# Kernel tuning notes

Measured on AMD Instinct MI355X. Metric: run time of the kernel, lower is better.

## Reference

```python
import jax, jax.numpy as jnp
import numpy as np

B = 8192      # graphs per batch
NPG = 40      # nodes per graph (= average_nodes, uniform here)
DEG = 16      # avg degree
IN = 64
HID = 32
OUT = 10
K1 = 20       # ceil(0.5*40)
K2 = 10       # ceil(0.5*20)
N = B * NPG
E = N * DEG
EPS = 1e-15


def _lin_params(k, fi, fo):
    kw, kb = jax.random.split(k)
    s = 1.0 / np.sqrt(fi)
    w = jax.random.uniform(kw, (fi, fo), jnp.float32, -s, s)
    b = jax.random.uniform(kb, (fo,), jnp.float32, -s, s)
    return w, b


def setup_inputs():
    key = jax.random.key(0)
    ks = jax.random.split(key, 14)
    x = jax.random.normal(ks[0], (N, IN), jnp.float32)
    # edges constrained within each graph (graphs are contiguous blocks of NPG nodes)
    g = jnp.repeat(jnp.arange(B, dtype=jnp.int32), NPG * DEG)
    src = g * NPG + jax.random.randint(ks[1], (E,), 0, NPG, dtype=jnp.int32)
    dst = g * NPG + jax.random.randint(ks[2], (E,), 0, NPG, dtype=jnp.int32)
    edge_index = jnp.stack([src, dst])
    batch = jnp.repeat(jnp.arange(B, dtype=jnp.int32), NPG)
    w_c1, b_c1 = _lin_params(ks[3], IN, HID)
    w_p1, b_p1 = _lin_params(ks[4], HID, K1)
    w2r, b2 = _lin_params(ks[5], HID, HID)
    w2o, _ = _lin_params(ks[6], HID, HID)
    w_p2, b_p2 = _lin_params(ks[7], HID, K2)
    w3r, b3 = _lin_params(ks[8], HID, HID)
    w3o, _ = _lin_params(ks[9], HID, HID)
    w_l1, b_l1 = _lin_params(ks[10], HID, HID)
    w_l2, b_l2 = _lin_params(ks[11], HID, OUT)
    return dict(x=x, edge_index=edge_index, batch=batch,
                w_c1=w_c1, b_c1=b_c1, w_p1=w_p1, b_p1=b_p1,
                w2r=w2r, b2=b2, w2o=w2o, w_p2=w_p2, b_p2=b_p2,
                w3r=w3r, b3=b3, w3o=w3o,
                w_l1=w_l1, b_l1=b_l1, w_l2=w_l2, b_l2=b_l2)


def _gcn_conv(x, edge_index, w, b):
    # PyG GCNConv: x' = D^-1/2 (A + I) D^-1/2 (X W) + b, unit edge weights
    h = x @ w
    row, col = edge_index
    deg = jnp.zeros((N,), h.dtype).at[col].add(1.0) + 1.0  # +1 self loop
    dinv = jax.lax.rsqrt(deg)
    msg = (dinv[row] * dinv[col])[:, None] * h[row]
    out = jnp.zeros_like(h).at[col].add(msg)
    out = out + (dinv * dinv)[:, None] * h  # self-loop contribution
    return out + b


def _dense_mincut_pool(x, adj, s, mask=None):
    # faithful to torch_geometric.nn.dense_mincut_pool
    s = jax.nn.softmax(s, axis=-1)
    if mask is not None:
        m = mask[..., None].astype(x.dtype)
        x = x * m
        s = s * m
    k = s.shape[-1]
    out = jnp.einsum('bnk,bnf->bkf', s, x)
    out_adj = jnp.einsum('bnk,bnm,bml->bkl', s, adj, s)
    mincut_num = jnp.trace(out_adj, axis1=1, axis2=2)
    d_flat = adj.sum(-1)                                   # [B, n]
    mincut_den = jnp.einsum('bnk,bn,bnk->b', s, d_flat, s)  # tr(S^T D S)
    mincut_loss = jnp.mean(-(mincut_num / mincut_den))
    ss = jnp.einsum('bnk,bnl->bkl', s, s)
    ss_norm = jnp.sqrt(jnp.sum(ss * ss, axis=(1, 2), keepdims=True))
    i_s = jnp.eye(k, dtype=x.dtype) / jnp.sqrt(jnp.asarray(k, x.dtype))
    ortho_loss = jnp.mean(jnp.sqrt(jnp.sum((ss / ss_norm - i_s) ** 2, axis=(1, 2))))
    # zero diagonal, then symmetric degree-normalize coarse adjacency
    eye = jnp.eye(k, dtype=x.dtype)
    out_adj = out_adj * (1.0 - eye)
    d = jnp.sqrt(out_adj.sum(-1))[:, None, :] + EPS        # [B,1,k]
    out_adj = out_adj / d / jnp.swapaxes(d, 1, 2)
    return out, out_adj, mincut_loss, ortho_loss


def _dense_graph_conv(x, adj, w_rel, b, w_root):
    # PyG DenseGraphConv (aggr='add'): lin_rel(A @ x) + lin_root(x); lin_root bias=False
    return (adj @ x) @ w_rel + b + x @ w_root


def reference(x, edge_index, batch, w_c1, b_c1, w_p1, b_p1, w2r, b2, w2o,
              w_p2, b_p2, w3r, b3, w3o, w_l1, b_l1, w_l2, b_l2):
    h = jax.nn.relu(_gcn_conv(x, edge_index, w_c1, b_c1))
    # to_dense_batch (uniform NPG nodes per graph, batch sorted)
    local = jnp.arange(N, dtype=jnp.int32) - batch * NPG
    xd = jnp.zeros((B, NPG, HID), h.dtype).at[batch, local].set(h)
    mask = jnp.ones((B, NPG), bool)
    # to_dense_adj (accumulates duplicate edges)
    row, col = edge_index
    g = batch[row]
    adj = jnp.zeros((B, NPG, NPG), h.dtype).at[g, row - g * NPG, col - g * NPG].add(1.0)
    s = xd @ w_p1 + b_p1
    xd, adj, mc1, o1 = _dense_mincut_pool(xd, adj, s, mask)
    xd = jax.nn.relu(_dense_graph_conv(xd, adj, w2r, b2, w2o))
    s = xd @ w_p2 + b_p2
    xd, adj, mc2, o2 = _dense_mincut_pool(xd, adj, s)
    xd = _dense_graph_conv(xd, adj, w3r, b3, w3o)
    pooled = xd.mean(axis=1)
    out = jax.nn.relu(pooled @ w_l1 + b_l1) @ w_l2 + b_l2
    return out, mc1 + mc2 + o1 + o2
```

## Files before the change

### kernel.cpp

```cpp
#include <hip/hip_runtime.h>

#define NT 256

constexpr int Bg   = 8192;
constexpr int NPG  = 40;
constexpr int EPG  = 640;
constexpr int IN_  = 64;
constexpr int HID  = 32;
constexpr int K1   = 20;
constexpr int K2   = 10;
constexpr int OUTC = 10;
constexpr int NE   = Bg * NPG * 16;
constexpr int SX   = 68;
constexpr int SH   = 36;

#define FMA4(acc, a, b) do { \
    acc.x = fmaf((a), (b).x, acc.x); \
    acc.y = fmaf((a), (b).y, acc.y); \
    acc.z = fmaf((a), (b).z, acc.z); \
    acc.w = fmaf((a), (b).w, acc.w); } while (0)

__device__ __forceinline__ float wave_red(float v) {
#pragma unroll
    for (int off = 32; off > 0; off >>= 1) v += __shfl_down(v, off, 64);
    return v;
}

__global__ __launch_bounds__(NT, 4)
void mincut_fused(const float* __restrict__ x, const int* __restrict__ ei,
                  const float* __restrict__ w_c1, const float* __restrict__ b_c1,
                  const float* __restrict__ w_p1, const float* __restrict__ b_p1,
                  const float* __restrict__ w2r_, const float* __restrict__ b2_,
                  const float* __restrict__ w2o_,
                  const float* __restrict__ w_p2, const float* __restrict__ b_p2,
                  const float* __restrict__ w3r_, const float* __restrict__ b3_,
                  const float* __restrict__ w3o_,
                  const float* __restrict__ w_l1, const float* __restrict__ b_l1,
                  const float* __restrict__ w_l2, const float* __restrict__ b_l2,
                  float* __restrict__ out, float* __restrict__ wsg)
{
    __shared__ __align__(16) float sXbuf[NPG * SX];
    __shared__ __align__(16) float sH[NPG * SH];
    __shared__ __align__(16) float sXd[NPG * SH];
    __shared__ __align__(16) float sA[NPG * NPG];
    __shared__ __align__(16) float sA2[K1 * K1];
    __shared__ __align__(16) float sX2[K1 * SH];
    __shared__ __align__(16) float sS2[K1 * K2];
    __shared__ __align__(16) float sX3[K2 * SH];
    __shared__ __align__(16) float sB1[HID];
    __shared__ __align__(16) float sBp1[K1];
    __shared__ __align__(16) float sB2[HID];
    __shared__ __align__(16) float sBp2[K2 + 2];
    __shared__ __align__(16) float sB3[HID];
    __shared__ __align__(16) float sdinv[NPG];
    __shared__ __align__(16) float srowsA[NPG];
    __shared__ __align__(16) float srowm[NPG];
    __shared__ __align__(16) float spool[HID];
    __shared__ __align__(16) float st1[HID];
    __shared__ __align__(16) float sred[4];
    __shared__ __align__(16) float sc[8];

    float* sS  = sXbuf;
    float* sAS = sXbuf + 800;
    float* sSS = sXbuf + 1600;
    float* sA3 = sXbuf + 2000;

    const int g    = blockIdx.x;
    const int tid  = threadIdx.x;
    const int lane = tid & 63;
    const int wid  = tid >> 6;

    int er0, ec0, er1, ec1, er2 = -1, ec2 = 0;
    {
        const int eb = g * EPG, nb = g * NPG;
        const int* srcp = ei;
        const int* dstp = ei + NE;
        int e = eb + tid;
        er0 = srcp[e] - nb; ec0 = dstp[e] - nb;
        e += NT;
        er1 = srcp[e] - nb; ec1 = dstp[e] - nb;
        if (tid + 2 * NT < EPG) {
            e += NT;
            er2 = srcp[e] - nb; ec2 = dstp[e] - nb;
        }
    }
    for (int i = tid; i < NPG * NPG; i += NT) sA[i] = 0.f;
    {
        const float4* xg = (const float4*)(x + (size_t)g * (NPG * IN_));
        for (int i = tid; i < NPG * (IN_ / 4); i += NT) {
            int n = i >> 4, k = i & 15;
            ((float4*)(sXbuf + n * SX))[k] = xg[i];
        }
    }
    if (tid < HID) { sB1[tid] = b_c1[tid]; sB2[tid] = b2_[tid]; sB3[tid] = b3_[tid]; }
    else if (tid >= 64 && tid < 64 + K1)   sBp1[tid - 64]  = b_p1[tid - 64];
    else if (tid >= 128 && tid < 128 + K2) sBp2[tid - 128] = b_p2[tid - 128];
    __syncthreads();

    atomicAdd(&sA[er0 * NPG + ec0], 1.f);
    atomicAdd(&sA[er1 * NPG + ec1], 1.f);
    if (er2 >= 0) atomicAdd(&sA[er2 * NPG + ec2], 1.f);

    if (tid < 160) {
        int np = tid >> 3, fq = tid & 7;
        int n0 = 2 * np, n1 = n0 + 1;
        const float4* a0p = (const float4*)(sXbuf + n0 * SX);
        const float4* a1p = (const float4*)(sXbuf + n1 * SX);
        const float4* wg  = (const float4*)w_c1;
        float4 acc0 = {0.f,0.f,0.f,0.f}, acc1 = {0.f,0.f,0.f,0.f};
#pragma unroll 4
        for (int kk = 0; kk < IN_ / 4; kk++) {
            float4 a0 = a0p[kk], a1 = a1p[kk];
            float4 w0 = wg[(4*kk+0)*8 + fq];
            float4 w1 = wg[(4*kk+1)*8 + fq];
            float4 w2 = wg[(4*kk+2)*8 + fq];
            float4 w3 = wg[(4*kk+3)*8 + fq];
            FMA4(acc0, a0.x, w0); FMA4(acc0, a0.y, w1);
            FMA4(acc0, a0.z, w2); FMA4(acc0, a0.w, w3);
            FMA4(acc1, a1.x, w0); FMA4(acc1, a1.y, w1);
            FMA4(acc1, a1.z, w2); FMA4(acc1, a1.w, w3);
        }
        ((float4*)(sH + n0 * SH))[fq] = acc0;
        ((float4*)(sH + n1 * SH))[fq] = acc1;
    }
    __syncthreads();

    if (tid < NPG) {
        float s = 0.f;
#pragma unroll
        for (int r = 0; r < NPG; r++) s += sA[r * NPG + tid];
        sdinv[tid] = rsqrtf(s + 1.f);
    } else if (tid >= 64 && tid < 64 + NPG) {
        int n = tid - 64; float s = 0.f;
#pragma unroll
        for (int m = 0; m < NPG; m++) s += sA[n * NPG + m];
        srowsA[n] = s;
    }
    __syncthreads();

    if (tid < 160) {
        int cp = tid >> 3, fq = tid & 7;
        int c0 = 2 * cp, c1 = c0 + 1;
        float4 acc0 = {0.f,0.f,0.f,0.f}, acc1 = {0.f,0.f,0.f,0.f};
#pragma unroll 8
        for (int r = 0; r < NPG; r++) {
            float dv = sdinv[r];
            float a0 = sA[r * NPG + c0] * dv;
            float a1 = sA[r * NPG + c1] * dv;
            float4 b = ((const float4*)(sH + r * SH))[fq];
            FMA4(acc0, a0, b);
            FMA4(acc1, a1, b);
        }
        float4 bb = ((const float4*)sB1)[fq];
        float4 h0 = ((const float4*)(sH + c0 * SH))[fq];
        float4 h1 = ((const float4*)(sH + c1 * SH))[fq];
        float d0 = sdinv[c0], d1 = sdinv[c1];
        float4 r0, r1;
        r0.x = fmaxf(fmaf(d0, fmaf(d0, h0.x, acc0.x), bb.x), 0.f);
        r0.y = fmaxf(fmaf(d0, fmaf(d0, h0.y, acc0.y), bb.y), 0.f);
        r0.z = fmaxf(fmaf(d0, fmaf(d0, h0.z, acc0.z), bb.z), 0.f);
        r0.w = fmaxf(fmaf(d0, fmaf(d0, h0.w, acc0.w), bb.w), 0.f);
        r1.x = fmaxf(fmaf(d1, fmaf(d1, h1.x, acc1.x), bb.x), 0.f);
        r1.y = fmaxf(fmaf(d1, fmaf(d1, h1.y, acc1.y), bb.y), 0.f);
        r1.z = fmaxf(fmaf(d1, fmaf(d1, h1.z, acc1.z), bb.z), 0.f);
        r1.w = fmaxf(fmaf(d1, fmaf(d1, h1.w, acc1.w), bb.w), 0.f);
        ((float4*)(sXd + c0 * SH))[fq] = r0;
        ((float4*)(sXd + c1 * SH))[fq] = r1;
    }
    __syncthreads();

    if (tid < 100) {
        int np = tid / 5, lq = tid - np * 5;
        int n0 = 2 * np, n1 = n0 + 1;
        const float4* wg = (const float4*)w_p1;
        float4 bb = ((const float4*)sBp1)[lq];
        float4 acc0 = bb, acc1 = bb;
#pragma unroll 8
        for (int k = 0; k < HID; k++) {
            float a0 = sXd[n0 * SH + k];
            float a1 = sXd[n1 * SH + k];
            float4 w = wg[k * 5 + lq];
            FMA4(acc0, a0, w);
            FMA4(acc1, a1, w);
        }
        ((float4*)(sS + n0 * K1))[lq] = acc0;
        ((float4*)(sS + n1 * K1))[lq] = acc1;
    }
    __syncthreads();

    if (tid < NPG) {
        float* row = sS + tid * K1;
        float v[K1]; float m = -3.0e38f;
#pragma unroll
        for (int k = 0; k < K1; k++) { v[k] = row[k]; m = fmaxf(m, v[k]); }
        float ssum = 0.f;
#pragma unroll
        for (int k = 0; k < K1; k++) { v[k] = __expf(v[k] - m); ssum += v[k]; }
        float inv = 1.f / ssum;
#pragma unroll
        for (int k = 0; k < K1; k++) row[k] = v[k] * inv;
    }
    __syncthreads();

    if (tid < 150) {
        if (tid < 100) {
            int np = tid / 5, lq = tid - np * 5;
            int n0 = 2 * np, n1 = n0 + 1;
            float4 acc0 = {0.f,0.f,0.f,0.f}, acc1 = {0.f,0.f,0.f,0.f};
#pragma unroll 8
            for (int m = 0; m < NPG; m++) {
                float a0 = sA[n0 * NPG + m];
                float a1 = sA[n1 * NPG + m];
                float4 b = ((const float4*)(sS + m * K1))[lq];
                FMA4(acc0, a0, b);
                FMA4(acc1, a1, b);
            }
            ((float4*)(sAS + n0 * K1))[lq] = acc0;
            ((float4*)(sAS + n1 * K1))[lq] = acc1;
        } else {
            int oo = tid - 100;
            int kp = oo / 5, lq = oo - kp * 5;
            int k0 = 2 * kp, k1 = k0 + 1;
            float4 acc0 = {0.f,0.f,0.f,0.f}, acc1 = {0.f,0.f,0.f,0.f};
#pragma unroll 8
            for (int n = 0; n < NPG; n++) {
                float s0 = sS[n * K1 + k0];
                float s1 = sS[n * K1 + k1];
                float4 b = ((const float4*)(sS + n * K1))[lq];
                FMA4(acc0, s0, b);
                FMA4(acc1, s1, b);
            }
            ((float4*)(sSS + k0 * K1))[lq] = acc0;
            ((float4*)(sSS + k1 * K1))[lq] = acc1;
        }
    }
    __syncthreads();

    if (tid < 170) {
        if (tid < 50) {
            int kp = tid / 5, lq = tid - kp * 5;
            int k0 = 2 * kp, k1 = k0 + 1;
            float4 acc0 = {0.f,0.f,0.f,0.f}, acc1 = {0.f,0.f,0.f,0.f};
#pragma unroll 8
            for (int n = 0; n < NPG; n++) {
                float s0 = sS[n * K1 + k0];
                float s1 = sS[n * K1 + k1];
                float4 b = ((const float4*)(sAS + n * K1))[lq];
                FMA4(acc0, s0, b);
                FMA4(acc1, s1, b);
            }
            ((float4*)(sA2 + k0 * K1))[lq] = acc0;
            ((float4*)(sA2 + k1 * K1))[lq] = acc1;
        } else if (tid < 130) {
            int oo = tid - 50;
            int kp = oo >> 3, fq = oo & 7;
            int k0 = 2 * kp, k1 = k0 + 1;
            float4 acc0 = {0.f,0.f,0.f,0.f}, acc1 = {0.f,0.f,0.f,0.f};
#pragma unroll 8
            for (int n = 0; n < NPG; n++) {
                float s0 = sS[n * K1 + k0];
                float s1 = sS[n * K1 + k1];
                float4 b = ((const float4*)(sXd + n * SH))[fq];
                FMA4(acc0, s0, b);
                FMA4(acc1, s1, b);
            }
            ((float4*)(sX2 + k0 * SH))[fq] = acc0;
            ((float4*)(sX2 + k1 * SH))[fq] = acc1;
        } else {
            int n = tid - 130;
            float s2 = 0.f;
#pragma unroll
            for (int k = 0; k < K1; k++) { float v = sS[n * K1 + k]; s2 = fmaf(v, v, s2); }
            srowm[n] = srowsA[n] * s2;
        }
    }
    __syncthreads();

    if (wid == 0) {
        float v = (lane < K1) ? sA2[lane * K1 + lane] : 0.f;
        v = wave_red(v); if (lane == 0) sc[0] = v;
    } else if (wid == 1) {
        float v = (lane < NPG) ? srowm[lane] : 0.f;
        v = wave_red(v); if (lane == 0) sc[1] = v;
    } else if (wid == 2) {
        float v = 0.f;
        for (int i = lane; i < K1 * K1; i += 64) { float t = sSS[i]; v = fmaf(t, t, v); }
        v = wave_red(v); if (lane == 0) sc[2] = v;
    }
    __syncthreads();

    {
        float rn = 1.f / sqrtf(sc[2]);
        const float isk = 0.22360679774997896f;
        float p = 0.f;
        for (int o = tid; o < K1 * K1; o += NT) {
            int k = o / K1, l = o - k * K1;
            float v = sSS[o] * rn - ((k == l) ? isk : 0.f);
            p = fmaf(v, v, p);
        }
        if (tid < K1) sA2[tid * K1 + tid] = 0.f;
        p = wave_red(p);
        if (lane == 0) sred[wid] = p;
    }
    __syncthreads();
    if (tid == 0) sc[3] = sred[0] + sred[1] + sred[2] + sred[3];
    if (tid < K1) {
        float s = 0.f;
#pragma unroll
        for (int l = 0; l < K1; l++) s += sA2[tid * K1 + l];
        srowm[tid] = 1.f / (sqrtf(s) + 1e-15f);
    }
    __syncthreads();

    for (int o = tid; o < 480; o += NT) {
        if (o < 400) {
            int k = o / K1, l = o - k * K1;
            sA2[o] *= srowm[k] * srowm[l];
        } else {
            int oo = o - 400;
            int kp = oo >> 3, fq = oo & 7;
            int k0 = 2 * kp, k1 = k0 + 1;
            const float4* wg = (const float4*)w2o_;
            float4 acc0 = {0.f,0.f,0.f,0.f}, acc1 = {0.f,0.f,0.f,0.f};
#pragma unroll 4
            for (int j = 0; j < HID; j++) {
                float a0 = sX2[k0 * SH + j];
                float a1 = sX2[k1 * SH + j];
                float4 w = wg[j * 8 + fq];
                FMA4(acc0, a0, w);
                FMA4(acc1, a1, w);
            }
            ((float4*)(sXd + k0 * SH))[fq] = acc0;
            ((float4*)(sXd + k1 * SH))[fq] = acc1;
        }
    }
    __syncthreads();

    if (tid < 80) {
        int kp = tid >> 3, fq = tid & 7;
        int k0 = 2 * kp, k1 = k0 + 1;
        float4 acc0 = {0.f,0.f,0.f,0.f}, acc1 = {0.f,0.f,0.f,0.f};
#pragma unroll
        for (int l = 0; l < K1; l++) {
            float a0 = sA2[k0 * K1 + l];
            float a1 = sA2[k1 * K1 + l];
            float4 b = ((const float4*)(sX2 + l * SH))[fq];
            FMA4(acc0, a0, b);
            FMA4(acc1, a1, b);
        }
        ((float4*)(sAS + k0 * SH))[fq] = acc0;
        ((float4*)(sAS + k1 * SH))[fq] = acc1;
    }
    __syncthreads();

    if (tid < 80) {
        int kp = tid >> 3, fq = tid & 7;
        int k0 = 2 * kp, k1 = k0 + 1;
        const float4* wg = (const float4*)w2r_;
        float4 bb = ((const float4*)sB2)[fq];
        float4 acc0 = ((const float4*)(sXd + k0 * SH))[fq];
        float4 acc1 = ((const float4*)(sXd + k1 * SH))[fq];
        acc0.x += bb.x; acc0.y += bb.y; acc0.z += bb.z; acc0.w += bb.w;
        acc1.x += bb.x; acc1.y += bb.y; acc1.z += bb.z; acc1.w += bb.w;
#pragma unroll 4
        for (int j = 0; j < HID; j++) {
            float a0 = sAS[k0 * SH + j];
            float a1 = sAS[k1 * SH + j];
            float4 w = wg[j * 8 + fq];
            FMA4(acc0, a0, w);
            FMA4(acc1, a1, w);
        }
        acc0.x = fmaxf(acc0.x, 0.f); acc0.y = fmaxf(acc0.y, 0.f);
        acc0.z = fmaxf(acc0.z, 0.f); acc0.w = fmaxf(acc0.w, 0.f);
        acc1.x = fmaxf(acc1.x, 0.f); acc1.y = fmaxf(acc1.y, 0.f);
        acc1.z = fmaxf(acc1.z, 0.f); acc1.w = fmaxf(acc1.w, 0.f);
        ((float4*)(sX2 + k0 * SH))[fq] = acc0;
        ((float4*)(sX2 + k1 * SH))[fq] = acc1;
    }
    __syncthreads();

    if (tid < K1 * K2) {
        int n = tid / K2, q = tid - n * K2;
        float acc = sBp2[q];
#pragma unroll 8
        for (int j = 0; j < HID; j++) acc = fmaf(sX2[n * SH + j], w_p2[j * K2 + q], acc);
        sS2[tid] = acc;
    }
    __syncthreads();
    if (tid < K1) {
        float* row = sS2 + tid * K2;
        float v[K2]; float m = -3.0e38f;
#pragma unroll
        for (int q = 0; q < K2; q++) { v[q] = row[q]; m = fmaxf(m, v[q]); }
        float ssum = 0.f;
#pragma unroll
        for (int q = 0; q < K2; q++) { v[q] = __expf(v[q] - m); ssum += v[q]; }
        float inv = 1.f / ssum;
#pragma unroll
        for (int q = 0; q < K2; q++) row[q] = v[q] * inv;
    }
    __syncthreads();

    for (int o = tid; o < 400; o += NT) {
        if (o < 200) {
            int n = o / K2, l = o - n * K2;
            float acc = 0.f;
#pragma unroll
            for (int m = 0; m < K1; m++) acc = fmaf(sA2[n * K1 + m], sS2[m * K2 + l], acc);
            sAS[n * K2 + l] = acc;
        } else if (o < 300) {
            int oo = o - 200; int k = oo / K2, l = oo - k * K2;
            float acc = 0.f;
#pragma unroll
            for (int n = 0; n < K1; n++) acc = fmaf(sS2[n * K2 + k], sS2[n * K2 + l], acc);
            sSS[k * K2 + l] = acc;
        } else if (o < 380) {
            int oo = o - 300; int k = oo >> 3, fq = oo & 7;
            float4 acc = {0.f, 0.f, 0.f, 0.f};
#pragma unroll
            for (int n = 0; n < K1; n++) {
                float a = sS2[n * K2 + k];
                float4 b = ((const float4*)(sX2 + n * SH))[fq];
                FMA4(acc, a, b);
            }
            ((float4*)(sX3 + k * SH))[fq] = acc;
        } else {
            int n = o - 380;
            float da = 0.f, s2 = 0.f;
#pragma unroll
            for (int l = 0; l < K1; l++) da += sA2[n * K1 + l];
#pragma unroll
            for (int q = 0; q < K2; q++) { float v = sS2[n * K2 + q]; s2 = fmaf(v, v, s2); }
            srowm[n] = da * s2;
        }
    }
    __syncthreads();

    if (tid < K2 * K2) {
        int k = tid / K2, l = tid - k * K2;
        float acc = 0.f;
#pragma unroll
        for (int n = 0; n < K1; n++) acc = fmaf(sS2[n * K2 + k], sAS[n * K2 + l], acc);
        sA3[tid] = acc;
    }
    __syncthreads();

    if (wid == 0) {
        float v = (lane < K2) ? sA3[lane * K2 + lane] : 0.f;
        v = wave_red(v); if (lane == 0) sc[4] = v;
    } else if (wid == 1) {
        float v = (lane < K1) ? srowm[lane] : 0.f;
        v = wave_red(v); if (lane == 0) sc[5] = v;
    } else if (wid == 2) {
        float v = 0.f;
        for (int i = lane; i < K2 * K2; i += 64) { float t = sSS[i]; v = fmaf(t, t, v); }
        v = wave_red(v); if (lane == 0) sc[6] = v;
    }
    __syncthreads();

    {
        float rn = 1.f / sqrtf(sc[6]);
        const float isk = 0.31622776601683794f;
        float p = 0.f;
        if (tid < K2 * K2) {
            int k = tid / K2, l = tid - k * K2;
            float v = sSS[tid] * rn - ((k == l) ? isk : 0.f);
            p = fmaf(v, v, p);
        }
        if (tid < K2) sA3[tid * K2 + tid] = 0.f;
        p = wave_red(p);
        if (lane == 0) sred[wid] = p;
    }
    __syncthreads();
    if (tid == 0) {
        float o2 = sqrtf(sred[0] + sred[1] + sred[2] + sred[3]);
        float loss = -(sc[0] / sc[1]) + sqrtf(sc[3]) - (sc[4] / sc[5]) + o2;
        wsg[g] = loss;
    }
    if (tid < K2) {
        float s = 0.f;
#pragma unroll
        for (int l = 0; l < K2; l++) s += sA3[tid * K2 + l];
        srowm[tid] = 1.f / (sqrtf(s) + 1e-15f);
    }
    __syncthreads();

    if (tid < 140) {
        if (tid < 100) {
            int k = tid / K2, l = tid - k * K2;
            sA3[tid] *= srowm[k] * srowm[l];
        } else {
            int oo = tid - 100;
            int kp = oo >> 3, fq = oo & 7;
            int k0 = 2 * kp, k1 = k0 + 1;
            const float4* wg = (const float4*)w3o_;
            float4 acc0 = {0.f,0.f,0.f,0.f}, acc1 = {0.f,0.f,0.f,0.f};
#pragma unroll 4
            for (int j = 0; j < HID; j++) {
                float a0 = sX3[k0 * SH + j];
                float a1 = sX3[k1 * SH + j];
                float4 w = wg[j * 8 + fq];
                FMA4(acc0, a0, w);
                FMA4(acc1, a1, w);
            }
            ((float4*)(sXd + k0 * SH))[fq] = acc0;
            ((float4*)(sXd + k1 * SH))[fq] = acc1;
        }
    }
    __syncthreads();

    if (tid < 40) {
        int kp = tid >> 3, fq = tid & 7;
        int k0 = 2 * kp, k1 = k0 + 1;
        float4 acc0 = {0.f,0.f,0.f,0.f}, acc1 = {0.f,0.f,0.f,0.f};
#pragma unroll
        for (int l = 0; l < K2; l++) {
            float a0 = sA3[k0 * K2 + l];
            float a1 = sA3[k1 * K2 + l];
            float4 b = ((const float4*)(sX3 + l * SH))[fq];
            FMA4(acc0, a0, b);
            FMA4(acc1, a1, b);
        }
        ((float4*)(sAS + k0 * SH))[fq] = acc0;
        ((float4*)(sAS + k1 * SH))[fq] = acc1;
    }
    __syncthreads();

    if (tid < 40) {
        int kp = tid >> 3, fq = tid & 7;
        int k0 = 2 * kp, k1 = k0 + 1;
        const float4* wg = (const float4*)w3r_;
        float4 bb = ((const float4*)sB3)[fq];
        float4 acc0 = ((const float4*)(sXd + k0 * SH))[fq];
        float4 acc1 = ((const float4*)(sXd + k1 * SH))[fq];
        acc0.x += bb.x; acc0.y += bb.y; acc0.z += bb.z; acc0.w += bb.w;
        acc1.x += bb.x; acc1.y += bb.y; acc1.z += bb.z; acc1.w += bb.w;
#pragma unroll 4
        for (int j = 0; j < HID; j++) {
            float a0 = sAS[k0 * SH + j];
            float a1 = sAS[k1 * SH + j];
            float4 w = wg[j * 8 + fq];
            FMA4(acc0, a0, w);
            FMA4(acc1, a1, w);
        }
        ((float4*)(sX3 + k0 * SH))[fq] = acc0;
        ((float4*)(sX3 + k1 * SH))[fq] = acc1;
    }
    __syncthreads();

    if (tid < HID) {
        float s = 0.f;
#pragma unroll
        for (int n = 0; n < K2; n++) s += sX3[n * SH + tid];
        spool[tid] = s * (1.f / K2);
    }
    __syncthreads();
    if (tid < HID) {
        float acc = b_l1[tid];
#pragma unroll 8
        for (int j = 0; j < HID; j++) acc = fmaf(spool[j], w_l1[j * HID + tid], acc);
        st1[tid] = fmaxf(acc, 0.f);
    }
    __syncthreads();
    if (tid < OUTC) {
        float acc = b_l2[tid];
#pragma unroll 8
        for (int j = 0; j < HID; j++) acc = fmaf(st1[j], w_l2[j * OUTC + tid], acc);
        out[(size_t)g * OUTC + tid] = acc;
    }
}

__global__ void loss_reduce(const float* __restrict__ wsg, float* __restrict__ out)
{
    __shared__ float sred[4];
    int tid = threadIdx.x;
    float s = 0.f;
    for (int i = tid; i < Bg; i += NT) s += wsg[i];
    s = wave_red(s);
    if ((tid & 63) == 0) sred[tid >> 6] = s;
    __syncthreads();
    if (tid == 0) out[(size_t)Bg * OUTC] = (sred[0] + sred[1] + sred[2] + sred[3]) * (1.f / Bg);
}

extern "C" void kernel_launch(void* const* d_in, const int* in_sizes, int n_in,
                              void* d_out, int out_size, void* d_ws, size_t ws_size,
                              hipStream_t stream)
{
    const float* x    = (const float*)d_in[0];
    const int*   ei   = (const int*)  d_in[1];
    const float* w_c1 = (const float*)d_in[3];
    const float* b_c1 = (const float*)d_in[4];
    const float* w_p1 = (const float*)d_in[5];
    const float* b_p1 = (const float*)d_in[6];
    const float* w2r  = (const float*)d_in[7];
    const float* b2   = (const float*)d_in[8];
    const float* w2o  = (const float*)d_in[9];
    const float* w_p2 = (const float*)d_in[10];
    const float* b_p2 = (const float*)d_in[11];
    const float* w3r  = (const float*)d_in[12];
    const float* b3   = (const float*)d_in[13];
    const float* w3o  = (const float*)d_in[14];
    const float* w_l1 = (const float*)d_in[15];
    const float* b_l1 = (const float*)d_in[16];
    const float* w_l2 = (const float*)d_in[17];
    const float* b_l2 = (const float*)d_in[18];
    float* out = (float*)d_out;
    float* wsg = (float*)d_ws;

    hipLaunchKernelGGL(mincut_fused, dim3(Bg), dim3(NT), 0, stream,
                       x, ei, w_c1, b_c1, w_p1, b_p1, w2r, b2, w2o,
                       w_p2, b_p2, w3r, b3, w3o, w_l1, b_l1, w_l2, b_l2,
                       out, wsg);
    hipLaunchKernelGGL(loss_reduce, dim3(1), dim3(NT), 0, stream, wsg, out);
}
```

Before: 264.3 us.

## Restructure fused MinCut kernel to cut shared memory, barriers and normalization passes

```diff
diff --git a/kernel.cpp b/kernel.cpp
--- a/kernel.cpp
+++ b/kernel.cpp
@@ -11,14 +11,15 @@
 constexpr int K2   = 10;
 constexpr int OUTC = 10;
 constexpr int NE   = Bg * NPG * 16;
-constexpr int SX   = 68;
 constexpr int SH   = 36;
+constexpr float EPSF = 1e-15f;
 
 #define FMA4(acc, a, b) do { \
-    acc.x = fmaf((a), (b).x, acc.x); \
-    acc.y = fmaf((a), (b).y, acc.y); \
-    acc.z = fmaf((a), (b).z, acc.z); \
-    acc.w = fmaf((a), (b).w, acc.w); } while (0)
+    float _s = (a); \
+    acc.x = fmaf(_s, (b).x, acc.x); \
+    acc.y = fmaf(_s, (b).y, acc.y); \
+    acc.z = fmaf(_s, (b).z, acc.z); \
+    acc.w = fmaf(_s, (b).w, acc.w); } while (0)
 
 __device__ __forceinline__ float wave_red(float v) {
 #pragma unroll
@@ -26,7 +27,7 @@
     return v;
 }
 
-__global__ __launch_bounds__(NT, 4)
+__global__ __launch_bounds__(NT, 6)
 void mincut_fused(const float* __restrict__ x, const int* __restrict__ ei,
                   const float* __restrict__ w_c1, const float* __restrict__ b_c1,
                   const float* __restrict__ w_p1, const float* __restrict__ b_p1,
@@ -39,31 +40,32 @@
                   const float* __restrict__ w_l2, const float* __restrict__ b_l2,
                   float* __restrict__ out, float* __restrict__ wsg)
 {
-    __shared__ __align__(16) float sXbuf[NPG * SX];
-    __shared__ __align__(16) float sH[NPG * SH];
-    __shared__ __align__(16) float sXd[NPG * SH];
-    __shared__ __align__(16) float sA[NPG * NPG];
-    __shared__ __align__(16) float sA2[K1 * K1];
-    __shared__ __align__(16) float sX2[K1 * SH];
-    __shared__ __align__(16) float sS2[K1 * K2];
-    __shared__ __align__(16) float sX3[K2 * SH];
-    __shared__ __align__(16) float sB1[HID];
-    __shared__ __align__(16) float sBp1[K1];
-    __shared__ __align__(16) float sB2[HID];
-    __shared__ __align__(16) float sBp2[K2 + 2];
-    __shared__ __align__(16) float sB3[HID];
+    __shared__ __align__(16) float sA_[NPG * NPG];
+    __shared__ __align__(16) float bufH[NPG * SH];
+    __shared__ __align__(16) float bufXd[NPG * SH];
+    __shared__ __align__(16) float bufS[NPG * K1];
+    __shared__ __align__(16) float bufAS[NPG * K1];
+    __shared__ __align__(16) float sSS[K1 * K1];
     __shared__ __align__(16) float sdinv[NPG];
     __shared__ __align__(16) float srowsA[NPG];
     __shared__ __align__(16) float srowm[NPG];
-    __shared__ __align__(16) float spool[HID];
-    __shared__ __align__(16) float st1[HID];
-    __shared__ __align__(16) float sred[4];
+    __shared__ __align__(16) float sden[NPG];
+    __shared__ __align__(16) float sred1[2];
+    __shared__ __align__(16) float sred2[2];
     __shared__ __align__(16) float sc[8];
 
-    float* sS  = sXbuf;
-    float* sAS = sXbuf + 800;
-    float* sSS = sXbuf + 1600;
-    float* sA3 = sXbuf + 2000;
+    float* sA2  = sA_;
+    float* sX2  = bufH;
+    float* sW2r = bufH + 720;
+    float* sW2o = bufAS;
+    float* sS2  = bufS;
+    float* sAS2 = bufS + 200;
+    float* sA3  = bufS + 400;
+    float* sSS2 = bufS + 500;
+    float* sW3r = bufXd;
+    float* sW3o = bufXd + 360;
+    float* sX3  = bufXd + 720;
+    float* sX4  = bufXd + 1080;
 
     const int g    = blockIdx.x;
     const int tid  = threadIdx.x;
@@ -84,33 +86,23 @@
             er2 = srcp[e] - nb; ec2 = dstp[e] - nb;
         }
     }
-    for (int i = tid; i < NPG * NPG; i += NT) sA[i] = 0.f;
-    {
-        const float4* xg = (const float4*)(x + (size_t)g * (NPG * IN_));
-        for (int i = tid; i < NPG * (IN_ / 4); i += NT) {
-            int n = i >> 4, k = i & 15;
-            ((float4*)(sXbuf + n * SX))[k] = xg[i];
-        }
-    }
-    if (tid < HID) { sB1[tid] = b_c1[tid]; sB2[tid] = b2_[tid]; sB3[tid] = b3_[tid]; }
-    else if (tid >= 64 && tid < 64 + K1)   sBp1[tid - 64]  = b_p1[tid - 64];
-    else if (tid >= 128 && tid < 128 + K2) sBp2[tid - 128] = b_p2[tid - 128];
-    __syncthreads();
-
-    atomicAdd(&sA[er0 * NPG + ec0], 1.f);
-    atomicAdd(&sA[er1 * NPG + ec1], 1.f);
-    if (er2 >= 0) atomicAdd(&sA[er2 * NPG + ec2], 1.f);
+    for (int i = tid; i < NPG * NPG; i += NT) sA_[i] = 0.f;
+    __syncthreads();
+
+    atomicAdd(&sA_[er0 * NPG + ec0], 1.f);
+    atomicAdd(&sA_[er1 * NPG + ec1], 1.f);
+    if (er2 >= 0) atomicAdd(&sA_[er2 * NPG + ec2], 1.f);
 
     if (tid < 160) {
         int np = tid >> 3, fq = tid & 7;
         int n0 = 2 * np, n1 = n0 + 1;
-        const float4* a0p = (const float4*)(sXbuf + n0 * SX);
-        const float4* a1p = (const float4*)(sXbuf + n1 * SX);
-        const float4* wg  = (const float4*)w_c1;
+        const float4* x0 = (const float4*)(x + (size_t)g * (NPG * IN_) + n0 * IN_);
+        const float4* x1 = (const float4*)(x + (size_t)g * (NPG * IN_) + n1 * IN_);
+        const float4* wg = (const float4*)w_c1;
         float4 acc0 = {0.f,0.f,0.f,0.f}, acc1 = {0.f,0.f,0.f,0.f};
 #pragma unroll 4
         for (int kk = 0; kk < IN_ / 4; kk++) {
-            float4 a0 = a0p[kk], a1 = a1p[kk];
+            float4 a0 = x0[kk], a1 = x1[kk];
             float4 w0 = wg[(4*kk+0)*8 + fq];
             float4 w1 = wg[(4*kk+1)*8 + fq];
             float4 w2 = wg[(4*kk+2)*8 + fq];
@@ -120,20 +112,20 @@
             FMA4(acc1, a1.x, w0); FMA4(acc1, a1.y, w1);
             FMA4(acc1, a1.z, w2); FMA4(acc1, a1.w, w3);
         }
-        ((float4*)(sH + n0 * SH))[fq] = acc0;
-        ((float4*)(sH + n1 * SH))[fq] = acc1;
+        ((float4*)(bufH + n0 * SH))[fq] = acc0;
+        ((float4*)(bufH + n1 * SH))[fq] = acc1;
     }
     __syncthreads();
 
     if (tid < NPG) {
         float s = 0.f;
 #pragma unroll
-        for (int r = 0; r < NPG; r++) s += sA[r * NPG + tid];
+        for (int r = 0; r < NPG; r++) s += sA_[r * NPG + tid];
         sdinv[tid] = rsqrtf(s + 1.f);
     } else if (tid >= 64 && tid < 64 + NPG) {
         int n = tid - 64; float s = 0.f;
 #pragma unroll
-        for (int m = 0; m < NPG; m++) s += sA[n * NPG + m];
+        for (int m = 0; m < NPG; m++) s += sA_[n * NPG + m];
         srowsA[n] = s;
     }
     __syncthreads();
@@ -144,16 +136,15 @@
         float4 acc0 = {0.f,0.f,0.f,0.f}, acc1 = {0.f,0.f,0.f,0.f};
 #pragma unroll 8
         for (int r = 0; r < NPG; r++) {
+            float2 a2 = *(const float2*)&sA_[r * NPG + c0];
             float dv = sdinv[r];
-            float a0 = sA[r * NPG + c0] * dv;
-            float a1 = sA[r * NPG + c1] * dv;
-            float4 b = ((const float4*)(sH + r * SH))[fq];
-            FMA4(acc0, a0, b);
-            FMA4(acc1, a1, b);
-        }
-        float4 bb = ((const float4*)sB1)[fq];
-        float4 h0 = ((const float4*)(sH + c0 * SH))[fq];
-        float4 h1 = ((const float4*)(sH + c1 * SH))[fq];
+            float4 b = ((const float4*)(bufH + r * SH))[fq];
+            FMA4(acc0, a2.x * dv, b);
+            FMA4(acc1, a2.y * dv, b);
+        }
+        float4 bb = ((const float4*)b_c1)[fq];
+        float4 h0 = ((const float4*)(bufH + c0 * SH))[fq];
+        float4 h1 = ((const float4*)(bufH + c1 * SH))[fq];
         float d0 = sdinv[c0], d1 = sdinv[c1];
         float4 r0, r1;
         r0.x = fmaxf(fmaf(d0, fmaf(d0, h0.x, acc0.x), bb.x), 0.f);
@@ -164,8 +155,8 @@
         r1.y = fmaxf(fmaf(d1, fmaf(d1, h1.y, acc1.y), bb.y), 0.f);
         r1.z = fmaxf(fmaf(d1, fmaf(d1, h1.z, acc1.z), bb.z), 0.f);
         r1.w = fmaxf(fmaf(d1, fmaf(d1, h1.w, acc1.w), bb.w), 0.f);
-        ((float4*)(sXd + c0 * SH))[fq] = r0;
-        ((float4*)(sXd + c1 * SH))[fq] = r1;
+        ((float4*)(bufXd + c0 * SH))[fq] = r0;
+        ((float4*)(bufXd + c1 * SH))[fq] = r1;
     }
     __syncthreads();
 
@@ -173,23 +164,23 @@
         int np = tid / 5, lq = tid - np * 5;
         int n0 = 2 * np, n1 = n0 + 1;
         const float4* wg = (const float4*)w_p1;
-        float4 bb = ((const float4*)sBp1)[lq];
+        float4 bb = ((const float4*)b_p1)[lq];
         float4 acc0 = bb, acc1 = bb;
 #pragma unroll 8
         for (int k = 0; k < HID; k++) {
-            float a0 = sXd[n0 * SH + k];
-            float a1 = sXd[n1 * SH + k];
+            float a0 = bufXd[n0 * SH + k];
+            float a1 = bufXd[n1 * SH + k];
             float4 w = wg[k * 5 + lq];
             FMA4(acc0, a0, w);
             FMA4(acc1, a1, w);
         }
-        ((float4*)(sS + n0 * K1))[lq] = acc0;
-        ((float4*)(sS + n1 * K1))[lq] = acc1;
+        ((float4*)(bufS + n0 * K1))[lq] = acc0;
+        ((float4*)(bufS + n1 * K1))[lq] = acc1;
     }
     __syncthreads();
 
     if (tid < NPG) {
-        float* row = sS + tid * K1;
+        float* row = bufS + tid * K1;
         float v[K1]; float m = -3.0e38f;
 #pragma unroll
         for (int k = 0; k < K1; k++) { v[k] = row[k]; m = fmaxf(m, v[k]); }
@@ -202,137 +193,121 @@
     }
     __syncthreads();
 
-    if (tid < 150) {
-        if (tid < 100) {
-            int np = tid / 5, lq = tid - np * 5;
-            int n0 = 2 * np, n1 = n0 + 1;
-            float4 acc0 = {0.f,0.f,0.f,0.f}, acc1 = {0.f,0.f,0.f,0.f};
-#pragma unroll 8
-            for (int m = 0; m < NPG; m++) {
-                float a0 = sA[n0 * NPG + m];
-                float a1 = sA[n1 * NPG + m];
-                float4 b = ((const float4*)(sS + m * K1))[lq];
-                FMA4(acc0, a0, b);
-                FMA4(acc1, a1, b);
-            }
-            ((float4*)(sAS + n0 * K1))[lq] = acc0;
-            ((float4*)(sAS + n1 * K1))[lq] = acc1;
-        } else {
-            int oo = tid - 100;
-            int kp = oo / 5, lq = oo - kp * 5;
-            int k0 = 2 * kp, k1 = k0 + 1;
-            float4 acc0 = {0.f,0.f,0.f,0.f}, acc1 = {0.f,0.f,0.f,0.f};
-#pragma unroll 8
-            for (int n = 0; n < NPG; n++) {
-                float s0 = sS[n * K1 + k0];
-                float s1 = sS[n * K1 + k1];
-                float4 b = ((const float4*)(sS + n * K1))[lq];
-                FMA4(acc0, s0, b);
-                FMA4(acc1, s1, b);
-            }
-            ((float4*)(sSS + k0 * K1))[lq] = acc0;
-            ((float4*)(sSS + k1 * K1))[lq] = acc1;
-        }
-    }
-    __syncthreads();
-
-    if (tid < 170) {
-        if (tid < 50) {
-            int kp = tid / 5, lq = tid - kp * 5;
-            int k0 = 2 * kp, k1 = k0 + 1;
-            float4 acc0 = {0.f,0.f,0.f,0.f}, acc1 = {0.f,0.f,0.f,0.f};
-#pragma unroll 8
-            for (int n = 0; n < NPG; n++) {
-                float s0 = sS[n * K1 + k0];
-                float s1 = sS[n * K1 + k1];
-                float4 b = ((const float4*)(sAS + n * K1))[lq];
-                FMA4(acc0, s0, b);
-                FMA4(acc1, s1, b);
-            }
-            ((float4*)(sA2 + k0 * K1))[lq] = acc0;
-            ((float4*)(sA2 + k1 * K1))[lq] = acc1;
-        } else if (tid < 130) {
-            int oo = tid - 50;
-            int kp = oo >> 3, fq = oo & 7;
-            int k0 = 2 * kp, k1 = k0 + 1;
-            float4 acc0 = {0.f,0.f,0.f,0.f}, acc1 = {0.f,0.f,0.f,0.f};
-#pragma unroll 8
-            for (int n = 0; n < NPG; n++) {
-                float s0 = sS[n * K1 + k0];
-                float s1 = sS[n * K1 + k1];
-                float4 b = ((const float4*)(sXd + n * SH))[fq];
-                FMA4(acc0, s0, b);
-                FMA4(acc1, s1, b);
-            }
-            ((float4*)(sX2 + k0 * SH))[fq] = acc0;
-            ((float4*)(sX2 + k1 * SH))[fq] = acc1;
-        } else {
-            int n = tid - 130;
-            float s2 = 0.f;
-#pragma unroll
-            for (int k = 0; k < K1; k++) { float v = sS[n * K1 + k]; s2 = fmaf(v, v, s2); }
-            srowm[n] = srowsA[n] * s2;
-        }
-    }
-    __syncthreads();
-
-    if (wid == 0) {
-        float v = (lane < K1) ? sA2[lane * K1 + lane] : 0.f;
-        v = wave_red(v); if (lane == 0) sc[0] = v;
-    } else if (wid == 1) {
-        float v = (lane < NPG) ? srowm[lane] : 0.f;
-        v = wave_red(v); if (lane == 0) sc[1] = v;
-    } else if (wid == 2) {
+    if (tid < 100) {
+        int np = tid / 5, lq = tid - np * 5;
+        int n0 = 2 * np, n1 = n0 + 1;
+        const float4* sb = (const float4*)bufS;
+        float4 acc0 = {0.f,0.f,0.f,0.f}, acc1 = {0.f,0.f,0.f,0.f};
+#pragma unroll
+        for (int m4 = 0; m4 < NPG / 4; m4++) {
+            float4 a0 = *(const float4*)&sA_[n0 * NPG + 4 * m4];
+            float4 a1 = *(const float4*)&sA_[n1 * NPG + 4 * m4];
+            float4 b0 = sb[(4*m4+0)*5 + lq];
+            float4 b1 = sb[(4*m4+1)*5 + lq];
+            float4 b2v = sb[(4*m4+2)*5 + lq];
+            float4 b3v = sb[(4*m4+3)*5 + lq];
+            FMA4(acc0, a0.x, b0); FMA4(acc0, a0.y, b1);
+            FMA4(acc0, a0.z, b2v); FMA4(acc0, a0.w, b3v);
+            FMA4(acc1, a1.x, b0); FMA4(acc1, a1.y, b1);
+            FMA4(acc1, a1.z, b2v); FMA4(acc1, a1.w, b3v);
+        }
+        ((float4*)(bufAS + n0 * K1))[lq] = acc0;
+        ((float4*)(bufAS + n1 * K1))[lq] = acc1;
+    } else if (tid < 150) {
+        int oo = tid - 100;
+        int kp = oo / 5, lq = oo - kp * 5;
+        int k0 = 2 * kp, k1 = k0 + 1;
+        float4 acc0 = {0.f,0.f,0.f,0.f}, acc1 = {0.f,0.f,0.f,0.f};
+#pragma unroll 8
+        for (int n = 0; n < NPG; n++) {
+            float2 s2v = *(const float2*)&bufS[n * K1 + k0];
+            float4 b = ((const float4*)(bufS + n * K1))[lq];
+            FMA4(acc0, s2v.x, b);
+            FMA4(acc1, s2v.y, b);
+        }
+        ((float4*)(sSS + k0 * K1))[lq] = acc0;
+        ((float4*)(sSS + k1 * K1))[lq] = acc1;
+    }
+    __syncthreads();
+
+    if (tid < 50) {
+        int kp = tid / 5, lq = tid - kp * 5;
+        int k0 = 2 * kp, k1 = k0 + 1;
+        float4 acc0 = {0.f,0.f,0.f,0.f}, acc1 = {0.f,0.f,0.f,0.f};
+#pragma unroll 8
+        for (int n = 0; n < NPG; n++) {
+            float2 s2v = *(const float2*)&bufS[n * K1 + k0];
+            float4 b = ((const float4*)(bufAS + n * K1))[lq];
+            FMA4(acc0, s2v.x, b);
+            FMA4(acc1, s2v.y, b);
+        }
+        ((float4*)(sA2 + k0 * K1))[lq] = acc0;
+        ((float4*)(sA2 + k1 * K1))[lq] = acc1;
+    } else if (tid < 130) {
+        int oo = tid - 50;
+        int kp = oo >> 3, fq = oo & 7;
+        int k0 = 2 * kp, k1 = k0 + 1;
+        float4 acc0 = {0.f,0.f,0.f,0.f}, acc1 = {0.f,0.f,0.f,0.f};
+#pragma unroll 8
+        for (int n = 0; n < NPG; n++) {
+            float2 s2v = *(const float2*)&bufS[n * K1 + k0];
+            float4 b = ((const float4*)(bufXd + n * SH))[fq];
+            FMA4(acc0, s2v.x, b);
+            FMA4(acc1, s2v.y, b);
+        }
+        ((float4*)(sX2 + k0 * SH))[fq] = acc0;
+        ((float4*)(sX2 + k1 * SH))[fq] = acc1;
+    } else if (tid < 170) {
+        int n = tid - 130;
+        float s2 = 0.f;
+#pragma unroll
+        for (int k = 0; k < K1; k++) { float v = bufS[n * K1 + k]; s2 = fmaf(v, v, s2); }
+        sden[n] = srowsA[n] * s2;
+    } else if (wid == 3) {
         float v = 0.f;
         for (int i = lane; i < K1 * K1; i += 64) { float t = sSS[i]; v = fmaf(t, t, v); }
         v = wave_red(v); if (lane == 0) sc[2] = v;
     }
     __syncthreads();
 
-    {
+    if (wid < 2) {
         float rn = 1.f / sqrtf(sc[2]);
         const float isk = 0.22360679774997896f;
         float p = 0.f;
-        for (int o = tid; o < K1 * K1; o += NT) {
+        for (int o = tid; o < K1 * K1; o += 128) {
             int k = o / K1, l = o - k * K1;
             float v = sSS[o] * rn - ((k == l) ? isk : 0.f);
             p = fmaf(v, v, p);
         }
-        if (tid < K1) sA2[tid * K1 + tid] = 0.f;
         p = wave_red(p);
-        if (lane == 0) sred[wid] = p;
-    }
-    __syncthreads();
-    if (tid == 0) sc[3] = sred[0] + sred[1] + sred[2] + sred[3];
-    if (tid < K1) {
-        float s = 0.f;
-#pragma unroll
-        for (int l = 0; l < K1; l++) s += sA2[tid * K1 + l];
-        srowm[tid] = 1.f / (sqrtf(s) + 1e-15f);
-    }
-    __syncthreads();
-
-    for (int o = tid; o < 480; o += NT) {
-        if (o < 400) {
-            int k = o / K1, l = o - k * K1;
-            sA2[o] *= srowm[k] * srowm[l];
-        } else {
-            int oo = o - 400;
-            int kp = oo >> 3, fq = oo & 7;
-            int k0 = 2 * kp, k1 = k0 + 1;
-            const float4* wg = (const float4*)w2o_;
-            float4 acc0 = {0.f,0.f,0.f,0.f}, acc1 = {0.f,0.f,0.f,0.f};
-#pragma unroll 4
-            for (int j = 0; j < HID; j++) {
-                float a0 = sX2[k0 * SH + j];
-                float a1 = sX2[k1 * SH + j];
-                float4 w = wg[j * 8 + fq];
-                FMA4(acc0, a0, w);
-                FMA4(acc1, a1, w);
-            }
-            ((float4*)(sXd + k0 * SH))[fq] = acc0;
-            ((float4*)(sXd + k1 * SH))[fq] = acc1;
-        }
+        if (lane == 0) sred1[wid] = p;
+    } else if (wid == 2) {
+        float v = (lane < K1) ? sA2[lane * (K1 + 1)] : 0.f;
+        v = wave_red(v); if (lane == 0) sc[0] = v;
+        if (lane < K1) {
+            float s = 0.f;
+#pragma unroll
+            for (int l = 0; l < K1; l++) s += sA2[lane * K1 + l];
+            s -= sA2[lane * (K1 + 1)];
+            srowm[lane] = 1.f / (sqrtf(s) + EPSF);
+        }
+    } else {
+        float v = (lane < NPG) ? sden[lane] : 0.f;
+        v = wave_red(v); if (lane == 0) sc[1] = v;
+    }
+    for (int o = tid; o < 320; o += NT) {
+        bool first = (o < 160);
+        int oo = first ? o : o - 160;
+        int n = oo >> 3, fq = oo & 7;
+        const float4* wg = (const float4*)(first ? w2r_ : w2o_);
+        float4 acc = {0.f,0.f,0.f,0.f};
+#pragma unroll 8
+        for (int k = 0; k < HID; k++) {
+            float a = sX2[n * SH + k];
+            FMA4(acc, a, wg[k * 8 + fq]);
+        }
+        if (first) ((float4*)(sW2r + n * SH))[fq] = acc;
+        else       ((float4*)(sW2o + n * SH))[fq] = acc;
     }
     __syncthreads();
 
@@ -342,51 +317,40 @@
         float4 acc0 = {0.f,0.f,0.f,0.f}, acc1 = {0.f,0.f,0.f,0.f};
 #pragma unroll
         for (int l = 0; l < K1; l++) {
-            float a0 = sA2[k0 * K1 + l];
-            float a1 = sA2[k1 * K1 + l];
-            float4 b = ((const float4*)(sX2 + l * SH))[fq];
-            FMA4(acc0, a0, b);
-            FMA4(acc1, a1, b);
-        }
-        ((float4*)(sAS + k0 * SH))[fq] = acc0;
-        ((float4*)(sAS + k1 * SH))[fq] = acc1;
-    }
-    __syncthreads();
-
-    if (tid < 80) {
-        int kp = tid >> 3, fq = tid & 7;
-        int k0 = 2 * kp, k1 = k0 + 1;
-        const float4* wg = (const float4*)w2r_;
-        float4 bb = ((const float4*)sB2)[fq];
-        float4 acc0 = ((const float4*)(sXd + k0 * SH))[fq];
-        float4 acc1 = ((const float4*)(sXd + k1 * SH))[fq];
-        acc0.x += bb.x; acc0.y += bb.y; acc0.z += bb.z; acc0.w += bb.w;
-        acc1.x += bb.x; acc1.y += bb.y; acc1.z += bb.z; acc1.w += bb.w;
-#pragma unroll 4
-        for (int j = 0; j < HID; j++) {
-            float a0 = sAS[k0 * SH + j];
-            float a1 = sAS[k1 * SH + j];
-            float4 w = wg[j * 8 + fq];
-            FMA4(acc0, a0, w);
-            FMA4(acc1, a1, w);
-        }
-        acc0.x = fmaxf(acc0.x, 0.f); acc0.y = fmaxf(acc0.y, 0.f);
-        acc0.z = fmaxf(acc0.z, 0.f); acc0.w = fmaxf(acc0.w, 0.f);
-        acc1.x = fmaxf(acc1.x, 0.f); acc1.y = fmaxf(acc1.y, 0.f);
-        acc1.z = fmaxf(acc1.z, 0.f); acc1.w = fmaxf(acc1.w, 0.f);
-        ((float4*)(sX2 + k0 * SH))[fq] = acc0;
-        ((float4*)(sX2 + k1 * SH))[fq] = acc1;
+            float rl = srowm[l];
+            float a0 = (l == k0) ? 0.f : sA2[k0 * K1 + l];
+            float a1 = (l == k1) ? 0.f : sA2[k1 * K1 + l];
+            float4 w = ((const float4*)(sW2r + l * SH))[fq];
+            FMA4(acc0, a0 * rl, w);
+            FMA4(acc1, a1 * rl, w);
+        }
+        float4 bb = ((const float4*)b2_)[fq];
+        float4 o0 = ((const float4*)(sW2o + k0 * SH))[fq];
+        float4 o1 = ((const float4*)(sW2o + k1 * SH))[fq];
+        float rk0 = srowm[k0], rk1 = srowm[k1];
+        float4 r0, r1;
+        r0.x = fmaxf(fmaf(rk0, acc0.x, o0.x + bb.x), 0.f);
+        r0.y = fmaxf(fmaf(rk0, acc0.y, o0.y + bb.y), 0.f);
+        r0.z = fmaxf(fmaf(rk0, acc0.z, o0.z + bb.z), 0.f);
+        r0.w = fmaxf(fmaf(rk0, acc0.w, o0.w + bb.w), 0.f);
+        r1.x = fmaxf(fmaf(rk1, acc1.x, o1.x + bb.x), 0.f);
+        r1.y = fmaxf(fmaf(rk1, acc1.y, o1.y + bb.y), 0.f);
+        r1.z = fmaxf(fmaf(rk1, acc1.z, o1.z + bb.z), 0.f);
+        r1.w = fmaxf(fmaf(rk1, acc1.w, o1.w + bb.w), 0.f);
+        ((float4*)(sX2 + k0 * SH))[fq] = r0;
+        ((float4*)(sX2 + k1 * SH))[fq] = r1;
     }
     __syncthreads();
 
     if (tid < K1 * K2) {
         int n = tid / K2, q = tid - n * K2;
-        float acc = sBp2[q];
+        float acc = b_p2[q];
 #pragma unroll 8
         for (int j = 0; j < HID; j++) acc = fmaf(sX2[n * SH + j], w_p2[j * K2 + q], acc);
         sS2[tid] = acc;
     }
     __syncthreads();
+
     if (tid < K1) {
         float* row = sS2 + tid * K2;
         float v[K2]; float m = -3.0e38f;
@@ -406,14 +370,17 @@
             int n = o / K2, l = o - n * K2;
             float acc = 0.f;
 #pragma unroll
-            for (int m = 0; m < K1; m++) acc = fmaf(sA2[n * K1 + m], sS2[m * K2 + l], acc);
-            sAS[n * K2 + l] = acc;
+            for (int m = 0; m < K1; m++) {
+                float a = (m == n) ? 0.f : sA2[n * K1 + m];
+                acc = fmaf(a * srowm[m], sS2[m * K2 + l], acc);
+            }
+            sAS2[n * K2 + l] = acc * srowm[n];
         } else if (o < 300) {
             int oo = o - 200; int k = oo / K2, l = oo - k * K2;
             float acc = 0.f;
 #pragma unroll
             for (int n = 0; n < K1; n++) acc = fmaf(sS2[n * K2 + k], sS2[n * K2 + l], acc);
-            sSS[k * K2 + l] = acc;
+            sSS2[k * K2 + l] = acc;
         } else if (o < 380) {
             int oo = o - 300; int k = oo >> 3, fq = oo & 7;
             float4 acc = {0.f, 0.f, 0.f, 0.f};
@@ -428,10 +395,14 @@
             int n = o - 380;
             float da = 0.f, s2 = 0.f;
 #pragma unroll
-            for (int l = 0; l < K1; l++) da += sA2[n * K1 + l];
+            for (int l = 0; l < K1; l++) {
+                float a = (l == n) ? 0.f : sA2[n * K1 + l];
+                da = fmaf(a, srowm[l], da);
+            }
+            da *= srowm[n];
 #pragma unroll
             for (int q = 0; q < K2; q++) { float v = sS2[n * K2 + q]; s2 = fmaf(v, v, s2); }
-            srowm[n] = da * s2;
+            sden[n] = da * s2;
         }
     }
     __syncthreads();
@@ -440,72 +411,59 @@
         int k = tid / K2, l = tid - k * K2;
         float acc = 0.f;
 #pragma unroll
-        for (int n = 0; n < K1; n++) acc = fmaf(sS2[n * K2 + k], sAS[n * K2 + l], acc);
+        for (int n = 0; n < K1; n++) acc = fmaf(sS2[n * K2 + k], sAS2[n * K2 + l], acc);
         sA3[tid] = acc;
+    } else if (wid == 2) {
+        float v = (lane < K1) ? sden[lane] : 0.f;
+        v = wave_red(v); if (lane == 0) sc[5] = v;
+    } else if (wid == 3) {
+        float v = 0.f;
+        for (int i = lane; i < K2 * K2; i += 64) { float t = sSS2[i]; v = fmaf(t, t, v); }
+        v = wave_red(v); if (lane == 0) sc[6] = v;
     }
     __syncthreads();
 
     if (wid == 0) {
-        float v = (lane < K2) ? sA3[lane * K2 + lane] : 0.f;
-        v = wave_red(v); if (lane == 0) sc[4] = v;
-    } else if (wid == 1) {
-        float v = (lane < K1) ? srowm[lane] : 0.f;
-        v = wave_red(v); if (lane == 0) sc[5] = v;
-    } else if (wid == 2) {
-        float v = 0.f;
-        for (int i = lane; i < K2 * K2; i += 64) { float t = sSS[i]; v = fmaf(t, t, v); }
-        v = wave_red(v); if (lane == 0) sc[6] = v;
-    }
-    __syncthreads();
-
-    {
         float rn = 1.f / sqrtf(sc[6]);
         const float isk = 0.31622776601683794f;
         float p = 0.f;
-        if (tid < K2 * K2) {
-            int k = tid / K2, l = tid - k * K2;
-            float v = sSS[tid] * rn - ((k == l) ? isk : 0.f);
+        for (int i = lane; i < K2 * K2; i += 64) {
+            int k = i / K2, l = i - k * K2;
+            float v = sSS2[i] * rn - ((k == l) ? isk : 0.f);
             p = fmaf(v, v, p);
         }
-        if (tid < K2) sA3[tid * K2 + tid] = 0.f;
         p = wave_red(p);
-        if (lane == 0) sred[wid] = p;
-    }
-    __syncthreads();
-    if (tid == 0) {
-        float o2 = sqrtf(sred[0] + sred[1] + sred[2] + sred[3]);
-        float loss = -(sc[0] / sc[1]) + sqrtf(sc[3]) - (sc[4] / sc[5]) + o2;
-        wsg[g] = loss;
-    }
-    if (tid < K2) {
-        float s = 0.f;
-#pragma unroll
-        for (int l = 0; l < K2; l++) s += sA3[tid * K2 + l];
-        srowm[tid] = 1.f / (sqrtf(s) + 1e-15f);
-    }
-    __syncthreads();
-
-    if (tid < 140) {
-        if (tid < 100) {
-            int k = tid / K2, l = tid - k * K2;
-            sA3[tid] *= srowm[k] * srowm[l];
-        } else {
-            int oo = tid - 100;
-            int kp = oo >> 3, fq = oo & 7;
-            int k0 = 2 * kp, k1 = k0 + 1;
-            const float4* wg = (const float4*)w3o_;
-            float4 acc0 = {0.f,0.f,0.f,0.f}, acc1 = {0.f,0.f,0.f,0.f};
-#pragma unroll 4
-            for (int j = 0; j < HID; j++) {
-                float a0 = sX3[k0 * SH + j];
-                float a1 = sX3[k1 * SH + j];
-                float4 w = wg[j * 8 + fq];
-                FMA4(acc0, a0, w);
-                FMA4(acc1, a1, w);
-            }
-            ((float4*)(sXd + k0 * SH))[fq] = acc0;
-            ((float4*)(sXd + k1 * SH))[fq] = acc1;
-        }
+        if (lane == 0) sred2[0] = p;
+    } else if (wid == 1) {
+        float v = (lane < K2) ? sA3[lane * (K2 + 1)] : 0.f;
+        v = wave_red(v); if (lane == 0) sc[4] = v;
+        if (lane < K2) {
+            float s = 0.f;
+#pragma unroll
+            for (int l = 0; l < K2; l++) s += sA3[lane * K2 + l];
+            s -= sA3[lane * (K2 + 1)];
+            srowm[lane] = 1.f / (sqrtf(s) + EPSF);
+        }
+    }
+    __syncthreads();
+
+    if (tid < 160) {
+        bool first = (tid < 80);
+        int oo = first ? tid : tid - 80;
+        int n = oo >> 3, fq = oo & 7;
+        const float4* wg = (const float4*)(first ? w3r_ : w3o_);
+        float4 acc = {0.f,0.f,0.f,0.f};
+#pragma unroll 8
+        for (int k = 0; k < HID; k++) {
+            float a = sX3[n * SH + k];
+            FMA4(acc, a, wg[k * 8 + fq]);
+        }
+        if (first) ((float4*)(sW3r + n * SH))[fq] = acc;
+        else       ((float4*)(sW3o + n * SH))[fq] = acc;
+    } else if (tid == 200) {
+        float o1 = sqrtf(sred1[0] + sred1[1]);
+        float o2 = sqrtf(sred2[0]);
+        wsg[g] = -(sc[0] / sc[1]) + o1 - (sc[4] / sc[5]) + o2;
     }
     __syncthreads();
 
@@ -515,58 +473,48 @@
         float4 acc0 = {0.f,0.f,0.f,0.f}, acc1 = {0.f,0.f,0.f,0.f};
 #pragma unroll
         for (int l = 0; l < K2; l++) {
-            float a0 = sA3[k0 * K2 + l];
-            float a1 = sA3[k1 * K2 + l];
-            float4 b = ((const float4*)(sX3 + l * SH))[fq];
-            FMA4(acc0, a0, b);
-            FMA4(acc1, a1, b);
-        }
-        ((float4*)(sAS + k0 * SH))[fq] = acc0;
-        ((float4*)(sAS + k1 * SH))[fq] = acc1;
-    }
-    __syncthreads();
-
-    if (tid < 40) {
-        int kp = tid >> 3, fq = tid & 7;
-        int k0 = 2 * kp, k1 = k0 + 1;
-        const float4* wg = (const float4*)w3r_;
-        float4 bb = ((const float4*)sB3)[fq];
-        float4 acc0 = ((const float4*)(sXd + k0 * SH))[fq];
-        float4 acc1 = ((const float4*)(sXd + k1 * SH))[fq];
-        acc0.x += bb.x; acc0.y += bb.y; acc0.z += bb.z; acc0.w += bb.w;
-        acc1.x += bb.x; acc1.y += bb.y; acc1.z += bb.z; acc1.w += bb.w;
-#pragma unroll 4
-        for (int j = 0; j < HID; j++) {
-            float a0 = sAS[k0 * SH + j];
-            float a1 = sAS[k1 * SH + j];
-            float4 w = wg[j * 8 + fq];
-            FMA4(acc0, a0, w);
-            FMA4(acc1, a1, w);
-        }
-        ((float4*)(sX3 + k0 * SH))[fq] = acc0;
-        ((float4*)(sX3 + k1 * SH))[fq] = acc1;
-    }
-    __syncthreads();
-
-    if (tid < HID) {
-        float s = 0.f;
-#pragma unroll
-        for (int n = 0; n < K2; n++) s += sX3[n * SH + tid];
-        spool[tid] = s * (1.f / K2);
-    }
-    __syncthreads();
-    if (tid < HID) {
-        float acc = b_l1[tid];
-#pragma unroll 8
-        for (int j = 0; j < HID; j++) acc = fmaf(spool[j], w_l1[j * HID + tid], acc);
-        st1[tid] = fmaxf(acc, 0.f);
-    }
-    __syncthreads();
-    if (tid < OUTC) {
-        float acc = b_l2[tid];
-#pragma unroll 8
-        for (int j = 0; j < HID; j++) acc = fmaf(st1[j], w_l2[j * OUTC + tid], acc);
-        out[(size_t)g * OUTC + tid] = acc;
+            float rl = srowm[l];
+            float a0 = (l == k0) ? 0.f : sA3[k0 * K2 + l];
+            float a1 = (l == k1) ? 0.f : sA3[k1 * K2 + l];
+            float4 w = ((const float4*)(sW3r + l * SH))[fq];
+            FMA4(acc0, a0 * rl, w);
+            FMA4(acc1, a1 * rl, w);
+        }
+        float4 bb = ((const float4*)b3_)[fq];
+        float4 o0 = ((const float4*)(sW3o + k0 * SH))[fq];
+        float4 o1 = ((const float4*)(sW3o + k1 * SH))[fq];
+        float rk0 = srowm[k0], rk1 = srowm[k1];
+        float4 r0, r1;
+        r0.x = fmaf(rk0, acc0.x, o0.x + bb.x);
+        r0.y = fmaf(rk0, acc0.y, o0.y + bb.y);
+        r0.z = fmaf(rk0, acc0.z, o0.z + bb.z);
+        r0.w = fmaf(rk0, acc0.w, o0.w + bb.w);
+        r1.x = fmaf(rk1, acc1.x, o1.x + bb.x);
+        r1.y = fmaf(rk1, acc1.y, o1.y + bb.y);
+        r1.z = fmaf(rk1, acc1.z, o1.z + bb.z);
+        r1.w = fmaf(rk1, acc1.w, o1.w + bb.w);
+        ((float4*)(sX4 + k0 * SH))[fq] = r0;
+        ((float4*)(sX4 + k1 * SH))[fq] = r1;
+    }
+    __syncthreads();
+
+    if (wid == 0) {
+        int f = lane & 31;
+        float pool = 0.f;
+#pragma unroll
+        for (int n = 0; n < K2; n++) pool += sX4[n * SH + f];
+        pool *= (1.f / K2);
+        float acc = b_l1[f];
+#pragma unroll
+        for (int j = 0; j < HID; j++)
+            acc = fmaf(__shfl(pool, j, 64), w_l1[j * HID + f], acc);
+        float t1 = fmaxf(acc, 0.f);
+        int o = (lane < OUTC) ? lane : 0;
+        float acc2 = b_l2[o];
+#pragma unroll
+        for (int j = 0; j < HID; j++)
+            acc2 = fmaf(__shfl(t1, j, 64), w_l2[j * OUTC + o], acc2);
+        if (lane < OUTC) out[(size_t)g * OUTC + lane] = acc2;
     }
 }
 
```

After: 384.9 us. 1.46x slower.
